# Kernel optimization log

Hardware: AMD Instinct MI355X
Metric: run time of the kernel (lower is better)

Reference implementation:

```python
import jax, jax.numpy as jnp
import numpy as np

N = 50000      # nodes
E = 800000     # edges (before self-loops)
G = 128        # graphs in batch
IN = 128       # in_channels
HID = 32       # hidden_channels (per head)
HEADS = 4
OUT = 64       # out_channels
SLOPE = 0.2    # PyG GATConv default negative_slope


def setup_inputs() -> dict:
    key = jax.random.key(0)
    ks = jax.random.split(key, 24)
    s = 0.1
    inp = {
        'x': jax.random.normal(ks[0], (N, IN), jnp.float32),
        'edge_index': jax.random.randint(ks[1], (2, E), 0, N, dtype=jnp.int32),
        'batch': jnp.sort(jax.random.randint(ks[2], (N,), 0, G, dtype=jnp.int32)),
        # conv1: IN -> HEADS*HID, concat
        'W1': jax.random.normal(ks[3], (IN, HEADS * HID), jnp.float32) * s,
        'a1s': jax.random.normal(ks[4], (HEADS, HID), jnp.float32) * s,
        'a1d': jax.random.normal(ks[5], (HEADS, HID), jnp.float32) * s,
        'b1': jnp.zeros((HEADS * HID,), jnp.float32),
        # conv2: HEADS*HID -> HEADS*HID, concat
        'W2': jax.random.normal(ks[6], (HEADS * HID, HEADS * HID), jnp.float32) * s,
        'a2s': jax.random.normal(ks[7], (HEADS, HID), jnp.float32) * s,
        'a2d': jax.random.normal(ks[8], (HEADS, HID), jnp.float32) * s,
        'b2': jnp.zeros((HEADS * HID,), jnp.float32),
        # conv3
        'W3': jax.random.normal(ks[9], (HEADS * HID, HEADS * HID), jnp.float32) * s,
        'a3s': jax.random.normal(ks[10], (HEADS, HID), jnp.float32) * s,
        'a3d': jax.random.normal(ks[11], (HEADS, HID), jnp.float32) * s,
        'b3': jnp.zeros((HEADS * HID,), jnp.float32),
        # conv4: heads=1, concat=False -> HID
        'W4': jax.random.normal(ks[12], (HEADS * HID, 1 * HID), jnp.float32) * s,
        'a4s': jax.random.normal(ks[13], (1, HID), jnp.float32) * s,
        'a4d': jax.random.normal(ks[14], (1, HID), jnp.float32) * s,
        'b4': jnp.zeros((HID,), jnp.float32),
        # fc: HID -> OUT
        'fcW': jax.random.normal(ks[15], (HID, OUT), jnp.float32) * s,
        'fcb': jnp.zeros((OUT,), jnp.float32),
    }
    return inp


def gat_conv(x, src, dst, W, a_src, a_dst, bias, heads, ch, concat):
    # x: [N, F_in]; src/dst: [E'] with self-loops (PyG add_self_loops=True)
    h = (x @ W).reshape(N, heads, ch)                       # [N, H, C]
    alpha_s = jnp.einsum('nhc,hc->nh', h, a_src)            # [N, H]
    alpha_d = jnp.einsum('nhc,hc->nh', h, a_dst)
    e = jax.nn.leaky_relu(alpha_s[src] + alpha_d[dst], SLOPE)  # [E', H]
    # segment softmax over edges grouped by destination node
    e_max = jax.ops.segment_max(e, dst, num_segments=N)
    e = jnp.exp(e - e_max[dst])
    denom = jax.ops.segment_sum(e, dst, num_segments=N)
    alpha = e / (denom[dst] + 1e-16)                        # [E', H]
    msg = h[src] * alpha[:, :, None]                        # [E', H, C]
    out = jax.ops.segment_sum(msg, dst, num_segments=N)     # [N, H, C]
    out = out.reshape(N, heads * ch) if concat else out.mean(axis=1)
    return out + bias


def reference(x, edge_index, batch, W1, a1s, a1d, b1, W2, a2s, a2d, b2,
              W3, a3s, a3d, b3, W4, a4s, a4d, b4, fcW, fcb):
    loop = jnp.arange(N, dtype=edge_index.dtype)
    src = jnp.concatenate([edge_index[0], loop])            # add self-loops once
    dst = jnp.concatenate([edge_index[1], loop])
    h = jax.nn.elu(gat_conv(x, src, dst, W1, a1s, a1d, b1, HEADS, HID, True))
    h = jax.nn.elu(gat_conv(h, src, dst, W2, a2s, a2d, b2, HEADS, HID, True))
    h = jax.nn.elu(gat_conv(h, src, dst, W3, a3s, a3d, b3, HEADS, HID, True))
    h = jax.nn.elu(gat_conv(h, src, dst, W4, a4s, a4d, b4, 1, HID, False))
    # global mean pool over graphs
    counts = jax.ops.segment_sum(jnp.ones((N,), h.dtype), batch, num_segments=G)
    pooled = jax.ops.segment_sum(h, batch, num_segments=G) / jnp.maximum(counts, 1.0)[:, None]
    # dropout p=0.5 is identity at inference
    return pooled @ fcW + fcb                               # [G, OUT]
```

## Files before the change

### kernel.cpp

```cpp
#include <hip/hip_runtime.h>


constexpr int NN     = 50000;
constexpr int NNPAD  = 50048;
constexpr int EE     = 800000;
constexpr int ETOT   = EE + NN;
constexpr int GG     = 128;
constexpr int HIDC   = 32;
constexpr int OUTC   = 64;

constexpr int NRANGE = (NN + 127) / 128;
constexpr int EPB    = 4096;
constexpr int NBLK   = (EE + EPB - 1) / EPB;
constexpr int RCAP   = 2688;

typedef short  bf16x8 __attribute__((ext_vector_type(8)));
typedef float  f32x4  __attribute__((ext_vector_type(4)));

static __device__ __forceinline__ unsigned short f2bf(float f) {
    unsigned int u = __float_as_uint(f);
    unsigned int r = (u + 0x7fffu + ((u >> 16) & 1u)) >> 16;
    return (unsigned short)r;
}
static __device__ __forceinline__ float bflo(unsigned int v) {
    return __uint_as_float(v << 16);
}
static __device__ __forceinline__ float bfhi(unsigned int v) {
    return __uint_as_float(v & 0xffff0000u);
}
static __device__ __forceinline__ float elu(float v) {
    return (v > 0.f) ? v : (__expf(v) - 1.f);
}
static __device__ __forceinline__ float leaky(float e) {
    return fmaxf(e, 0.f) + 0.2f * fminf(e, 0.f);
}

__global__ __launch_bounds__(256) void local_sort_kernel(
    const int* __restrict__ ei,
    unsigned int* __restrict__ blocksorted,
    int* __restrict__ boffs)
{
    __shared__ unsigned int sorted[EPB];
    __shared__ int hist[NRANGE + 1];
    __shared__ int scanv[NRANGE + 1];
    __shared__ int cur[NRANGE + 1];
    __shared__ int wsum4[4];
    __shared__ int ct_s;

    const int b = blockIdx.x, tid = threadIdx.x;
    const int lane = tid & 63, wid = tid >> 6;
    const int e0 = b * EPB;
    const int ecnt = min(EPB, EE - e0);

    for (int t = tid; t < NRANGE + 1; t += 256) hist[t] = 0;
    __syncthreads();

    unsigned int recs[16];
    int rkey[16];
#pragma unroll
    for (int k = 0; k < 16; ++k) {
        const int idx = tid + k * 256;
        rkey[k] = -1;
        if (idx < ecnt) {
            const int src = ei[e0 + idx];
            const int dst = ei[EE + e0 + idx];
            const int r = dst >> 7;
            recs[k] = (unsigned int)src | ((unsigned int)(dst & 127) << 16);
            rkey[k] = r;
            atomicAdd(&hist[r], 1);
        }
    }
    __syncthreads();

    int carry = 0;
    for (int base = 0; base < NRANGE + 1; base += 256) {
        const int i = base + tid;
        const int v = (i < NRANGE + 1) ? hist[i] : 0;
        int incl = v;
#pragma unroll
        for (int off = 1; off < 64; off <<= 1) {
            int t = __shfl_up(incl, off, 64);
            if (lane >= off) incl += t;
        }
        if (lane == 63) wsum4[wid] = incl;
        __syncthreads();
        if (tid == 0) {
            int s = 0;
#pragma unroll
            for (int w = 0; w < 4; ++w) { int t = wsum4[w]; wsum4[w] = s; s += t; }
            ct_s = s;
        }
        __syncthreads();
        const int excl = carry + wsum4[wid] + incl - v;
        if (i < NRANGE + 1) { scanv[i] = excl; cur[i] = excl; }
        carry += ct_s;
        __syncthreads();
    }

#pragma unroll
    for (int k = 0; k < 16; ++k) {
        if (rkey[k] >= 0) {
            const int pos = atomicAdd(&cur[rkey[k]], 1);
            sorted[pos] = recs[k];
        }
    }
    __syncthreads();

    for (int t = tid; t < ecnt; t += 256)
        blocksorted[(size_t)b * EPB + t] = sorted[t];
    for (int t = tid; t < NRANGE + 1; t += 256)
        boffs[b * (NRANGE + 1) + t] = scanv[t];
}

__global__ __launch_bounds__(256) void rtot_kernel(const int* __restrict__ boffs,
                                                   int* __restrict__ rtot)
{
    const int r = blockIdx.x * 4 + (threadIdx.x >> 6);
    const int lane = threadIdx.x & 63;
    if (r >= NRANGE) return;
    int tot = 0;
    for (int b = lane; b < NBLK; b += 64) {
        const int* bp = boffs + b * (NRANGE + 1) + r;
        tot += bp[1] - bp[0];
    }
#pragma unroll
    for (int k = 1; k < 64; k <<= 1) tot += __shfl_xor(tot, k, 64);
    if (lane == 0) rtot[r] = tot + min(128, NN - r * 128);
}

__global__ __launch_bounds__(512) void rscan_kernel(const int* __restrict__ rtot,
                                                    int* __restrict__ rbase)
{
    __shared__ int wsum[8], wpre[8];
    const int tid = threadIdx.x, lane = tid & 63, wid = tid >> 6;
    int tot = (tid < NRANGE) ? rtot[tid] : 0;
    int incl = tot;
#pragma unroll
    for (int off = 1; off < 64; off <<= 1) {
        int t = __shfl_up(incl, off, 64);
        if (lane >= off) incl += t;
    }
    if (lane == 63) wsum[wid] = incl;
    __syncthreads();
    if (tid < 8) {
        int wv = wsum[tid], winc = wv;
#pragma unroll
        for (int off = 1; off < 8; off <<= 1) {
            int t = __shfl_up(winc, off, 64);
            if (tid >= off) winc += t;
        }
        wpre[tid] = winc - wv;
    }
    __syncthreads();
    const int excl = wpre[wid] + incl - tot;
    if (tid < NRANGE) rbase[tid] = excl;
    if (tid == NRANGE - 1) rbase[NRANGE] = excl + tot;
}

__global__ __launch_bounds__(256) void phaseB_kernel(
    const int* __restrict__ boffs,
    const unsigned int* __restrict__ blocksorted,
    const int* __restrict__ rbase,
    int* __restrict__ offs,
    unsigned int* __restrict__ csrpack)
{
    __shared__ unsigned int rec[RCAP];
    __shared__ unsigned int outpk[RCAP];
    __shared__ int runoff[NBLK + 1];
    __shared__ int bstart[NBLK];
    __shared__ int hist[128], lofs[128], cur[128];
    __shared__ int wsum4[4];
    __shared__ int tot0_s;

    const int r = blockIdx.x, tid = threadIdx.x;
    const int lane = tid & 63, wid = tid >> 6;
    const int base = r * 128;
    const int rn   = min(128, NN - base);

    int cnt = 0;
    if (tid < NBLK) {
        const int* bp = boffs + tid * (NRANGE + 1) + r;
        const int s = bp[0];
        bstart[tid] = s;
        cnt = bp[1] - s;
    }
    if (tid < 128) hist[tid] = 0;
    int incl = cnt;
#pragma unroll
    for (int off = 1; off < 64; off <<= 1) {
        int t = __shfl_up(incl, off, 64);
        if (lane >= off) incl += t;
    }
    if (lane == 63) wsum4[wid] = incl;
    __syncthreads();
    if (tid == 0) {
        int s = 0;
#pragma unroll
        for (int w = 0; w < 4; ++w) { int t = wsum4[w]; wsum4[w] = s; s += t; }
    }
    __syncthreads();
    const int excl = wsum4[wid] + incl - cnt;
    if (tid <= NBLK) runoff[tid] = excl;
    __syncthreads();

    const int tot8 = runoff[NBLK];
    for (int i = tid; i < tot8; i += 256) {
        int lo = 0, hi = NBLK;
        while (lo + 1 < hi) {
            const int mid = (lo + hi) >> 1;
            if (runoff[mid] <= i) lo = mid; else hi = mid;
        }
        rec[i] = blocksorted[(size_t)lo * EPB + bstart[lo] + (i - runoff[lo])];
    }
    for (int t = tid; t < rn; t += 256)
        rec[tot8 + t] = (unsigned int)(base + t) | ((unsigned int)t << 16);
    const int total = min(tot8 + rn, RCAP);
    __syncthreads();

    for (int t = tid; t < total; t += 256) atomicAdd(&hist[rec[t] >> 16], 1);
    __syncthreads();

    if (tid < 64) {
        int v = hist[tid], incl2 = v;
#pragma unroll
        for (int off = 1; off < 64; off <<= 1) {
            int t = __shfl_up(incl2, off, 64);
            if (tid >= off) incl2 += t;
        }
        lofs[tid] = incl2 - v;
        if (tid == 63) tot0_s = incl2;
    }
    __syncthreads();
    if (tid >= 64 && tid < 128) {
        const int l = tid & 63;
        int v = hist[tid], incl2 = v;
#pragma unroll
        for (int off = 1; off < 64; off <<= 1) {
            int t = __shfl_up(incl2, off, 64);
            if (l >= off) incl2 += t;
        }
        lofs[tid] = tot0_s + incl2 - v;
    }
    __syncthreads();

    if (tid < 128) cur[tid] = lofs[tid];
    if (tid < rn) offs[base + tid] = rbase[r] + lofs[tid];
    if (r == 0 && tid == 0) offs[NN] = rbase[NRANGE];
    __syncthreads();

    for (int t = tid; t < total; t += 256) {
        const unsigned int rc = rec[t];
        const int pos = atomicAdd(&cur[rc >> 16], 1);
        outpk[pos] = (rc & 0xffffu) | ((unsigned int)(base + (rc >> 16)) << 16);
    }
    __syncthreads();
    const int rb = rbase[r];
    for (int t = tid; t < total; t += 256) csrpack[rb + t] = outpk[t];
}

__global__ __launch_bounds__(256) void prep_kernel(
    const float* __restrict__ W1, const float* __restrict__ a1s, const float* __restrict__ a1d,
    const float* __restrict__ W2, const float* __restrict__ a2s, const float* __restrict__ a2d,
    const float* __restrict__ W3, const float* __restrict__ a3s, const float* __restrict__ a3d,
    const float* __restrict__ W4, const float* __restrict__ a4s, const float* __restrict__ a4d,
    unsigned short* __restrict__ wtg)
{
    __shared__ float ahat_s[128 * 8];
    const int l = blockIdx.x, tid = threadIdx.x;
    const float *W, *as_, *ad_;
    int fo, nh;
    if (l == 0)      { W = W1; as_ = a1s; ad_ = a1d; fo = 128; nh = 4; }
    else if (l == 1) { W = W2; as_ = a2s; ad_ = a2d; fo = 128; nh = 4; }
    else if (l == 2) { W = W3; as_ = a3s; ad_ = a3d; fo = 128; nh = 4; }
    else             { W = W4; as_ = a4s; ad_ = a4d; fo = 32;  nh = 1; }
    const int F_STG = fo + 16;

    for (int item = tid; item < 128 * 8; item += 256) {
        const int k = item >> 3, j = item & 7;
        const int hh = j & 3;
        const bool is_d = j >= 4;
        float v = 0.f;
        if (hh < nh) {
            const float* av = (is_d ? ad_ : as_) + hh * 32;
            const float* wp = W + (size_t)k * fo + hh * 32;
#pragma unroll 8
            for (int c = 0; c < 32; ++c) v = fmaf(wp[c], av[c], v);
        }
        ahat_s[item] = v;
    }
    __syncthreads();

    unsigned short* outb = wtg + (size_t)l * (144 * 128);
    for (int p = tid; p < F_STG * 64; p += 256) {
        const int n  = p % F_STG;
        const int k2 = p / F_STG;
        float w0 = 0.f, w1 = 0.f;
        if (n < fo) {
            w0 = W[(size_t)(2 * k2) * fo + n];
            w1 = W[(size_t)(2 * k2 + 1) * fo + n];
        } else {
            const int j = n - fo;
            if (j < 8) {
                w0 = ahat_s[(2 * k2) * 8 + j];
                w1 = ahat_s[(2 * k2 + 1) * 8 + j];
            }
        }
        const unsigned int packed = (unsigned int)f2bf(w0) | ((unsigned int)f2bf(w1) << 16);
        const int byte = n * 256 + ((4 * k2) ^ ((n & 7) << 4));
        *reinterpret_cast<unsigned int*>(reinterpret_cast<char*>(outb) + byte) = packed;
    }
}

template<int F_OUT, int NH, bool XF32>
__global__ __launch_bounds__(256) void gemm_mfma_kernel(
    const void* __restrict__ xv,
    const unsigned short* __restrict__ wtg,
    unsigned short* __restrict__ hb,
    float* __restrict__ as_out, float* __restrict__ ad_out)
{
    constexpr int F_STG = F_OUT + 16;
    __shared__ unsigned short wt[F_STG * 128];
    const int tid = threadIdx.x;

    {
        const bf16x8* __restrict__ wg = reinterpret_cast<const bf16x8*>(wtg);
        bf16x8* wl = reinterpret_cast<bf16x8*>(wt);
        constexpr int NV = F_STG * 16;
#pragma unroll
        for (int i = 0; i < NV / 256; ++i)
            wl[i * 256 + tid] = wg[i * 256 + tid];
    }
    __syncthreads();

    const int wave = tid >> 6, lane = tid & 63;
    const int kchunk = (lane >> 4) * 8;
    const int kb_base = (lane >> 4) * 16;

#pragma unroll
    for (int rr = 0; rr < 2; ++rr) {
        const int row0 = blockIdx.x * 128 + rr * 64 + wave * 16;
        const int arow = row0 + (lane & 15);

        bf16x8 a[4];
        if (XF32) {
            if (arow < NN) {
                const float* __restrict__ ap = (const float*)xv + (size_t)arow * 128;
#pragma unroll
                for (int ks = 0; ks < 4; ++ks) {
                    const float4 f0 = *reinterpret_cast<const float4*>(ap + ks * 32 + kchunk);
                    const float4 f1 = *reinterpret_cast<const float4*>(ap + ks * 32 + kchunk + 4);
                    bf16x8 v;
                    v[0] = (short)f2bf(f0.x); v[1] = (short)f2bf(f0.y);
                    v[2] = (short)f2bf(f0.z); v[3] = (short)f2bf(f0.w);
                    v[4] = (short)f2bf(f1.x); v[5] = (short)f2bf(f1.y);
                    v[6] = (short)f2bf(f1.z); v[7] = (short)f2bf(f1.w);
                    a[ks] = v;
                }
            } else {
#pragma unroll
                for (int ks = 0; ks < 4; ++ks) a[ks] = bf16x8{0,0,0,0,0,0,0,0};
            }
        } else {
            const unsigned short* __restrict__ ap =
                (const unsigned short*)xv + (size_t)arow * 128;
#pragma unroll
            for (int ks = 0; ks < 4; ++ks)
                a[ks] = *reinterpret_cast<const bf16x8*>(ap + ks * 32 + kchunk);
        }

        const int rbase = row0 + (lane >> 4) * 4;

#pragma unroll
        for (int nt = 0; nt < F_OUT / 16; ++nt) {
            const int n = nt * 16 + (lane & 15);
            f32x4 acc = {0.f, 0.f, 0.f, 0.f};
#pragma unroll
            for (int ks = 0; ks < 4; ++ks) {
                const int byte = n * 256 + ((ks * 64 + kb_base) ^ ((n & 7) << 4));
                bf16x8 b = *reinterpret_cast<const bf16x8*>(
                    reinterpret_cast<const char*>(wt) + byte);
                acc = __builtin_amdgcn_mfma_f32_16x16x32_bf16(a[ks], b, acc, 0, 0, 0);
            }
#pragma unroll
            for (int r = 0; r < 4; ++r) {
                const int row = rbase + r;
                if (row < NN)
                    hb[(size_t)row * F_OUT + n] = f2bf(acc[r]);
            }
        }

        {
            const int n = F_OUT + (lane & 15);
            f32x4 acc = {0.f, 0.f, 0.f, 0.f};
#pragma unroll
            for (int ks = 0; ks < 4; ++ks) {
                const int byte = n * 256 + ((ks * 64 + kb_base) ^ ((n & 7) << 4));
                bf16x8 b = *reinterpret_cast<const bf16x8*>(
                    reinterpret_cast<const char*>(wt) + byte);
                acc = __builtin_amdgcn_mfma_f32_16x16x32_bf16(a[ks], b, acc, 0, 0, 0);
            }
            const int col = lane & 15;
            if (col < 8) {
                const int hh = col & 3;
                const bool is_d = col >= 4;
                if (hh < NH) {
                    float* op = is_d ? ad_out : as_out;
#pragma unroll
                    for (int r = 0; r < 4; ++r) {
                        const int row = rbase + r;
                        if (row < NN) {
                            if (NH == 4) op[row * 4 + hh] = acc[r];
                            else         op[row]          = acc[r];
                        }
                    }
                }
            }
        }
    }
}

template<int HEADS, int F_OUT, bool OUT_BF16>
__global__ __launch_bounds__(256) void aggregate_kernel(
    const unsigned short* __restrict__ hlin,
    const float* __restrict__ as_,
    const float* __restrict__ ad_,
    const int* __restrict__ offs,
    const unsigned int* __restrict__ csrpack,
    const float* __restrict__ bias,
    void* __restrict__ out_v)
{
    __shared__ float w_all[4][64 * HEADS];
    __shared__ int   s_all[4][64];
    const int wave = threadIdx.x >> 6;
    const int lane = threadIdx.x & 63;
    const int d    = blockIdx.x * 4 + wave;
    if (d >= NN) return;
    float* __restrict__ w_lds   = w_all[wave];
    int*   __restrict__ src_lds = s_all[wave];

    const int beg = offs[d], end = offs[d + 1];

    float ad_h[HEADS];
#pragma unroll
    for (int h = 0; h < HEADS; ++h) ad_h[h] = ad_[d * HEADS + h];

    float acc[8] = {0.f, 0.f, 0.f, 0.f, 0.f, 0.f, 0.f, 0.f};
    float dsum = 0.f;
    const int q  = (F_OUT == 128) ? (lane >> 4) : (lane >> 2);
    const int cl = (F_OUT == 128) ? (lane & 15) : (lane & 3);
    const int hd = (F_OUT == 128) ? (cl >> 2) : 0;

    for (int base = beg; base < end; base += 64) {
        const int cnt = min(64, end - base);
        {
            const int p = base + lane;
            unsigned int pk = (p < end) ? csrpack[p] : 0u;
            const int src = (int)(pk & 0xffffu);
            src_lds[lane] = src;
            if (HEADS == 4) {
                float4 w4 = make_float4(0.f, 0.f, 0.f, 0.f);
                if (p < end) {
                    const float4 s4 = *reinterpret_cast<const float4*>(
                        as_ + (size_t)src * 4);
                    w4.x = __expf(leaky(s4.x + ad_h[0]));
                    w4.y = __expf(leaky(s4.y + ad_h[1]));
                    w4.z = __expf(leaky(s4.z + ad_h[2]));
                    w4.w = __expf(leaky(s4.w + ad_h[3]));
                }
                *reinterpret_cast<float4*>(w_lds + lane * 4) = w4;
            } else {
                float w1 = 0.f;
                if (p < end) w1 = __expf(leaky(as_[src] + ad_h[0]));
                w_lds[lane] = w1;
            }
        }
        asm volatile("s_waitcnt lgkmcnt(0)" ::: "memory");

        if (F_OUT == 128) {
            const int cntR = (cnt + 3) & ~3;
#pragma unroll 2
            for (int j = 0; j < cntR; j += 4) {
                const int   slot = j + q;
                const int   srcj = src_lds[slot];
                const float w    = w_lds[slot * 4 + hd];
                const uint4 hv   = *reinterpret_cast<const uint4*>(
                    hlin + (size_t)srcj * 128 + cl * 8);
                dsum += w;
                acc[0] = fmaf(w, bflo(hv.x), acc[0]);
                acc[1] = fmaf(w, bfhi(hv.x), acc[1]);
                acc[2] = fmaf(w, bflo(hv.y), acc[2]);
                acc[3] = fmaf(w, bfhi(hv.y), acc[3]);
                acc[4] = fmaf(w, bflo(hv.z), acc[4]);
                acc[5] = fmaf(w, bfhi(hv.z), acc[5]);
                acc[6] = fmaf(w, bflo(hv.w), acc[6]);
                acc[7] = fmaf(w, bfhi(hv.w), acc[7]);
            }
        } else {
            const int cntR = (cnt + 15) & ~15;
#pragma unroll 2
            for (int j = 0; j < cntR; j += 16) {
                const int   slot = j + q;
                const int   srcj = src_lds[slot];
                const float w    = w_lds[slot];
                const uint4 hv   = *reinterpret_cast<const uint4*>(
                    hlin + (size_t)srcj * 32 + cl * 8);
                dsum += w;
                acc[0] = fmaf(w, bflo(hv.x), acc[0]);
                acc[1] = fmaf(w, bfhi(hv.x), acc[1]);
                acc[2] = fmaf(w, bflo(hv.y), acc[2]);
                acc[3] = fmaf(w, bfhi(hv.y), acc[3]);
                acc[4] = fmaf(w, bflo(hv.z), acc[4]);
                acc[5] = fmaf(w, bfhi(hv.z), acc[5]);
                acc[6] = fmaf(w, bflo(hv.w), acc[6]);
                acc[7] = fmaf(w, bfhi(hv.w), acc[7]);
            }
        }
    }

    if (F_OUT == 128) {
#pragma unroll
        for (int t = 0; t < 8; ++t) {
            acc[t] += __shfl_xor(acc[t], 16, 64);
            acc[t] += __shfl_xor(acc[t], 32, 64);
        }
        dsum += __shfl_xor(dsum, 16, 64);
        dsum += __shfl_xor(dsum, 32, 64);
        if (lane < 16) {
            const float rinv = 1.f / (dsum + 1e-16f);
            const int c0 = lane * 8;
            float v[8];
#pragma unroll
            for (int t = 0; t < 8; ++t) v[t] = elu(fmaf(acc[t], rinv, bias[c0 + t]));
            uint4 pk;
            pk.x = (unsigned int)f2bf(v[0]) | ((unsigned int)f2bf(v[1]) << 16);
            pk.y = (unsigned int)f2bf(v[2]) | ((unsigned int)f2bf(v[3]) << 16);
            pk.z = (unsigned int)f2bf(v[4]) | ((unsigned int)f2bf(v[5]) << 16);
            pk.w = (unsigned int)f2bf(v[6]) | ((unsigned int)f2bf(v[7]) << 16);
            *reinterpret_cast<uint4*>((unsigned short*)out_v + (size_t)d * 128 + c0) = pk;
        }
    } else {
#pragma unroll
        for (int t = 0; t < 8; ++t) {
            acc[t] += __shfl_xor(acc[t], 4, 64);
            acc[t] += __shfl_xor(acc[t], 8, 64);
            acc[t] += __shfl_xor(acc[t], 16, 64);
            acc[t] += __shfl_xor(acc[t], 32, 64);
        }
        dsum += __shfl_xor(dsum, 4, 64);
        dsum += __shfl_xor(dsum, 8, 64);
        dsum += __shfl_xor(dsum, 16, 64);
        dsum += __shfl_xor(dsum, 32, 64);
        if (lane < 4) {
            const float rinv = 1.f / (dsum + 1e-16f);
            const int c0 = lane * 8;
            float v[8];
#pragma unroll
            for (int t = 0; t < 8; ++t) v[t] = elu(fmaf(acc[t], rinv, bias[c0 + t]));
            float* op = (float*)out_v + (size_t)d * 32 + c0;
            *reinterpret_cast<float4*>(op)     = make_float4(v[0], v[1], v[2], v[3]);
            *reinterpret_cast<float4*>(op + 4) = make_float4(v[4], v[5], v[6], v[7]);
        }
    }
}

__global__ __launch_bounds__(256) void pool_fc_kernel(
    const float* __restrict__ h4, const int* __restrict__ batch,
    const float* __restrict__ fcW, const float* __restrict__ fcb,
    float* __restrict__ out)
{
    const int g = blockIdx.x;
    __shared__ int sb, se;
    if (threadIdx.x == 0) {
        int lo = 0, hi = NN;
        while (lo < hi) { int mid = (lo + hi) >> 1; if (batch[mid] < g) lo = mid + 1; else hi = mid; }
        sb = lo;
        lo = sb; hi = NN;
        while (lo < hi) { int mid = (lo + hi) >> 1; if (batch[mid] < g + 1) lo = mid + 1; else hi = mid; }
        se = lo;
    }
    __syncthreads();
    const int s = sb, e = se;

    const int c  = threadIdx.x & 31;
    const int rg = threadIdx.x >> 5;
    float acc = 0.f;
    for (int n = s + rg; n < e; n += 8)
        acc += h4[(size_t)n * HIDC + c];

    __shared__ float red[8][32];
    red[rg][c] = acc;
    __syncthreads();
    __shared__ float pooled_s[32];
    if (threadIdx.x < 32) {
        float v = 0.f;
#pragma unroll
        for (int r = 0; r < 8; ++r) v += red[r][threadIdx.x];
        pooled_s[threadIdx.x] = v / fmaxf((float)(e - s), 1.f);
    }
    __syncthreads();
    if (threadIdx.x < OUTC) {
        const int o = threadIdx.x;
        float a2 = fcb[o];
#pragma unroll
        for (int cc = 0; cc < HIDC; ++cc)
            a2 = fmaf(pooled_s[cc], fcW[cc * OUTC + o], a2);
        out[g * OUTC + o] = a2;
    }
}

extern "C" void kernel_launch(void* const* d_in, const int* in_sizes, int n_in,
                              void* d_out, int out_size, void* d_ws, size_t ws_size,
                              hipStream_t stream)
{
    const float* x     = (const float*)d_in[0];
    const int*   ei    = (const int*)d_in[1];
    const int*   batch = (const int*)d_in[2];
    const float* W1  = (const float*)d_in[3];
    const float* a1s = (const float*)d_in[4];
    const float* a1d = (const float*)d_in[5];
    const float* b1  = (const float*)d_in[6];
    const float* W2  = (const float*)d_in[7];
    const float* a2s = (const float*)d_in[8];
    const float* a2d = (const float*)d_in[9];
    const float* b2  = (const float*)d_in[10];
    const float* W3  = (const float*)d_in[11];
    const float* a3s = (const float*)d_in[12];
    const float* a3d = (const float*)d_in[13];
    const float* b3  = (const float*)d_in[14];
    const float* W4  = (const float*)d_in[15];
    const float* a4s = (const float*)d_in[16];
    const float* a4d = (const float*)d_in[17];
    const float* b4  = (const float*)d_in[18];
    const float* fcW = (const float*)d_in[19];
    const float* fcb = (const float*)d_in[20];
    float* out = (float*)d_out;

    unsigned short* xb = (unsigned short*)d_ws;
    unsigned short* hb = xb + (size_t)NNPAD * 128;
    float* asb  = (float*)(hb + (size_t)NNPAD * 128);
    float* adb  = asb + (size_t)NN * 4;
    int*   offs    = (int*)(adb + (size_t)NN * 4);
    unsigned int* csrpack = (unsigned int*)(offs + NN + 1);
    int*   boffs  = (int*)(csrpack + ETOT);
    int*   rbase  = boffs + NBLK * (NRANGE + 1);
    int*   rtot   = rbase + NRANGE + 1;
    unsigned short* wtg = (unsigned short*)(rtot + NRANGE);
    unsigned int* blocksorted = (unsigned int*)hb;
    float* bufF = (float*)xb;

    local_sort_kernel<<<NBLK, 256, 0, stream>>>(ei, blocksorted, boffs);
    rtot_kernel<<<(NRANGE + 3) / 4, 256, 0, stream>>>(boffs, rtot);
    rscan_kernel<<<1, 512, 0, stream>>>(rtot, rbase);
    phaseB_kernel<<<NRANGE, 256, 0, stream>>>(boffs, blocksorted, rbase, offs, csrpack);

    prep_kernel<<<4, 256, 0, stream>>>(W1, a1s, a1d, W2, a2s, a2d,
                                       W3, a3s, a3d, W4, a4s, a4d, wtg);

    constexpr int GEMM_GRID = NNPAD / 128;
    constexpr int AGG_GRID  = (NN + 3) / 4;
    constexpr size_t WSTRIDE = 144 * 128;

    gemm_mfma_kernel<128, 4, true><<<GEMM_GRID, 256, 0, stream>>>(x, wtg + 0 * WSTRIDE, hb, asb, adb);
    aggregate_kernel<4, 128, true><<<AGG_GRID, 256, 0, stream>>>(hb, asb, adb, offs, csrpack, b1, xb);
    gemm_mfma_kernel<128, 4, false><<<GEMM_GRID, 256, 0, stream>>>(xb, wtg + 1 * WSTRIDE, hb, asb, adb);
    aggregate_kernel<4, 128, true><<<AGG_GRID, 256, 0, stream>>>(hb, asb, adb, offs, csrpack, b2, xb);
    gemm_mfma_kernel<128, 4, false><<<GEMM_GRID, 256, 0, stream>>>(xb, wtg + 2 * WSTRIDE, hb, asb, adb);
    aggregate_kernel<4, 128, true><<<AGG_GRID, 256, 0, stream>>>(hb, asb, adb, offs, csrpack, b3, xb);
    gemm_mfma_kernel<32, 1, false><<<GEMM_GRID, 256, 0, stream>>>(xb, wtg + 3 * WSTRIDE, hb, asb, adb);
    aggregate_kernel<1, 32, false><<<AGG_GRID, 256, 0, stream>>>(hb, asb, adb, offs, csrpack, b4, bufF);

    pool_fc_kernel<<<GG, 256, 0, stream>>>(bufF, batch, fcW, fcb, out);
}
```

Before: 249.7 us.

## Process two destination nodes per wave in aggregation and use packed bf16 conversion

Each wave in the aggregate kernel now handles two destination nodes, interleaving their edge chunks so the gathers for both are in flight at once, and the grid shrinks to NN/8 blocks. The inner gather loop unroll goes from 2 to 4. Float-to-bf16 rounding now uses the HIP packed conversion intrinsic instead of manual bit arithmetic. The goal is more memory-level parallelism in the latency-bound gather. The cost is imbalance when the two nodes have different degrees, plus higher register pressure. The grid assumes NN is divisible by 8, and the d>=NN guard is removed.

Result: slower. 283.8 us (+13.7%).

```diff
diff --git a/kernel.cpp b/kernel.cpp
--- a/kernel.cpp
+++ b/kernel.cpp
@@ -1,4 +1,5 @@
 #include <hip/hip_runtime.h>
+#include <hip/hip_bf16.h>
 
 
 constexpr int NN     = 50000;
@@ -18,9 +19,12 @@
 typedef float  f32x4  __attribute__((ext_vector_type(4)));
 
 static __device__ __forceinline__ unsigned short f2bf(float f) {
-    unsigned int u = __float_as_uint(f);
-    unsigned int r = (u + 0x7fffu + ((u >> 16) & 1u)) >> 16;
-    return (unsigned short)r;
+    __hip_bfloat16 h = __float2bfloat16(f);
+    unsigned short u; __builtin_memcpy(&u, &h, 2); return u;
+}
+static __device__ __forceinline__ unsigned int f2bf2(float lo, float hi) {
+    __hip_bfloat162 h2 = __float22bfloat162_rn(make_float2(lo, hi));
+    unsigned int u; __builtin_memcpy(&u, &h2, 4); return u;
 }
 static __device__ __forceinline__ float bflo(unsigned int v) {
     return __uint_as_float(v << 16);
@@ -305,7 +309,7 @@
                 w1 = ahat_s[(2 * k2 + 1) * 8 + j];
             }
         }
-        const unsigned int packed = (unsigned int)f2bf(w0) | ((unsigned int)f2bf(w1) << 16);
+        const unsigned int packed = f2bf2(w0, w1);
         const int byte = n * 256 + ((4 * k2) ^ ((n & 7) << 4));
         *reinterpret_cast<unsigned int*>(reinterpret_cast<char*>(outb) + byte) = packed;
     }
@@ -349,11 +353,12 @@
                 for (int ks = 0; ks < 4; ++ks) {
                     const float4 f0 = *reinterpret_cast<const float4*>(ap + ks * 32 + kchunk);
                     const float4 f1 = *reinterpret_cast<const float4*>(ap + ks * 32 + kchunk + 4);
-                    bf16x8 v;
-                    v[0] = (short)f2bf(f0.x); v[1] = (short)f2bf(f0.y);
-                    v[2] = (short)f2bf(f0.z); v[3] = (short)f2bf(f0.w);
-                    v[4] = (short)f2bf(f1.x); v[5] = (short)f2bf(f1.y);
-                    v[6] = (short)f2bf(f1.z); v[7] = (short)f2bf(f1.w);
+                    uint4 u;
+                    u.x = f2bf2(f0.x, f0.y);
+                    u.y = f2bf2(f0.z, f0.w);
+                    u.z = f2bf2(f1.x, f1.y);
+                    u.w = f2bf2(f1.z, f1.w);
+                    bf16x8 v; __builtin_memcpy(&v, &u, 16);
                     a[ks] = v;
                 }
             } else {
@@ -419,6 +424,132 @@
     }
 }
 
+template<int HEADS>
+static __device__ __forceinline__ void agg_stage(
+    const unsigned int* __restrict__ csrpack, const float* __restrict__ as_,
+    const float* __restrict__ ad_h,
+    float* __restrict__ w_lds, int* __restrict__ src_lds,
+    int lane, int p0, int end)
+{
+    const int p = p0 + lane;
+    const unsigned int pk = (p < end) ? csrpack[p] : 0u;
+    const int src = (int)(pk & 0xffffu);
+    src_lds[lane] = src;
+    if (HEADS == 4) {
+        float4 w4 = make_float4(0.f, 0.f, 0.f, 0.f);
+        if (p < end) {
+            const float4 s4 = *reinterpret_cast<const float4*>(as_ + (size_t)src * 4);
+            w4.x = __expf(leaky(s4.x + ad_h[0]));
+            w4.y = __expf(leaky(s4.y + ad_h[1]));
+            w4.z = __expf(leaky(s4.z + ad_h[2]));
+            w4.w = __expf(leaky(s4.w + ad_h[3]));
+        }
+        *reinterpret_cast<float4*>(w_lds + lane * 4) = w4;
+    } else {
+        float w1 = 0.f;
+        if (p < end) w1 = __expf(leaky(as_[src] + ad_h[0]));
+        w_lds[lane] = w1;
+    }
+}
+
+template<int F_OUT>
+static __device__ __forceinline__ void agg_inner(
+    const unsigned short* __restrict__ hlin,
+    const float* __restrict__ w_lds, const int* __restrict__ src_lds,
+    int cnt, int q, int cl, int hd, float acc[8], float& dsum)
+{
+    if (F_OUT == 128) {
+        const int cntR = (cnt + 3) & ~3;
+#pragma unroll 4
+        for (int j = 0; j < cntR; j += 4) {
+            const int   slot = j + q;
+            const int   srcj = src_lds[slot];
+            const float w    = w_lds[slot * 4 + hd];
+            const uint4 hv   = *reinterpret_cast<const uint4*>(
+                hlin + (size_t)srcj * 128 + cl * 8);
+            dsum += w;
+            acc[0] = fmaf(w, bflo(hv.x), acc[0]);
+            acc[1] = fmaf(w, bfhi(hv.x), acc[1]);
+            acc[2] = fmaf(w, bflo(hv.y), acc[2]);
+            acc[3] = fmaf(w, bfhi(hv.y), acc[3]);
+            acc[4] = fmaf(w, bflo(hv.z), acc[4]);
+            acc[5] = fmaf(w, bfhi(hv.z), acc[5]);
+            acc[6] = fmaf(w, bflo(hv.w), acc[6]);
+            acc[7] = fmaf(w, bfhi(hv.w), acc[7]);
+        }
+    } else {
+        const int cntR = (cnt + 15) & ~15;
+#pragma unroll 4
+        for (int j = 0; j < cntR; j += 16) {
+            const int   slot = j + q;
+            const int   srcj = src_lds[slot];
+            const float w    = w_lds[slot];
+            const uint4 hv   = *reinterpret_cast<const uint4*>(
+                hlin + (size_t)srcj * 32 + cl * 8);
+            dsum += w;
+            acc[0] = fmaf(w, bflo(hv.x), acc[0]);
+            acc[1] = fmaf(w, bfhi(hv.x), acc[1]);
+            acc[2] = fmaf(w, bflo(hv.y), acc[2]);
+            acc[3] = fmaf(w, bfhi(hv.y), acc[3]);
+            acc[4] = fmaf(w, bflo(hv.z), acc[4]);
+            acc[5] = fmaf(w, bfhi(hv.z), acc[5]);
+            acc[6] = fmaf(w, bflo(hv.w), acc[6]);
+            acc[7] = fmaf(w, bfhi(hv.w), acc[7]);
+        }
+    }
+}
+
+template<int F_OUT, bool OUT_BF16>
+static __device__ __forceinline__ void agg_epilogue(
+    float acc[8], float dsum, int lane, int d,
+    const float* __restrict__ bias, void* __restrict__ out_v)
+{
+    if (F_OUT == 128) {
+#pragma unroll
+        for (int t = 0; t < 8; ++t) {
+            acc[t] += __shfl_xor(acc[t], 16, 64);
+            acc[t] += __shfl_xor(acc[t], 32, 64);
+        }
+        dsum += __shfl_xor(dsum, 16, 64);
+        dsum += __shfl_xor(dsum, 32, 64);
+        if (lane < 16) {
+            const float rinv = 1.f / (dsum + 1e-16f);
+            const int c0 = lane * 8;
+            float v[8];
+#pragma unroll
+            for (int t = 0; t < 8; ++t) v[t] = elu(fmaf(acc[t], rinv, bias[c0 + t]));
+            uint4 pk;
+            pk.x = f2bf2(v[0], v[1]);
+            pk.y = f2bf2(v[2], v[3]);
+            pk.z = f2bf2(v[4], v[5]);
+            pk.w = f2bf2(v[6], v[7]);
+            *reinterpret_cast<uint4*>((unsigned short*)out_v + (size_t)d * 128 + c0) = pk;
+        }
+    } else {
+#pragma unroll
+        for (int t = 0; t < 8; ++t) {
+            acc[t] += __shfl_xor(acc[t], 4, 64);
+            acc[t] += __shfl_xor(acc[t], 8, 64);
+            acc[t] += __shfl_xor(acc[t], 16, 64);
+            acc[t] += __shfl_xor(acc[t], 32, 64);
+        }
+        dsum += __shfl_xor(dsum, 4, 64);
+        dsum += __shfl_xor(dsum, 8, 64);
+        dsum += __shfl_xor(dsum, 16, 64);
+        dsum += __shfl_xor(dsum, 32, 64);
+        if (lane < 4) {
+            const float rinv = 1.f / (dsum + 1e-16f);
+            const int c0 = lane * 8;
+            float v[8];
+#pragma unroll
+            for (int t = 0; t < 8; ++t) v[t] = elu(fmaf(acc[t], rinv, bias[c0 + t]));
+            float* op = (float*)out_v + (size_t)d * 32 + c0;
+            *reinterpret_cast<float4*>(op)     = make_float4(v[0], v[1], v[2], v[3]);
+            *reinterpret_cast<float4*>(op + 4) = make_float4(v[4], v[5], v[6], v[7]);
+        }
+    }
+}
+
 template<int HEADS, int F_OUT, bool OUT_BF16>
 __global__ __launch_bounds__(256) void aggregate_kernel(
     const unsigned short* __restrict__ hlin,
@@ -429,138 +560,52 @@
     const float* __restrict__ bias,
     void* __restrict__ out_v)
 {
-    __shared__ float w_all[4][64 * HEADS];
-    __shared__ int   s_all[4][64];
+    __shared__ float w_all[8][64 * HEADS];
+    __shared__ int   s_all[8][64];
     const int wave = threadIdx.x >> 6;
     const int lane = threadIdx.x & 63;
-    const int d    = blockIdx.x * 4 + wave;
-    if (d >= NN) return;
-    float* __restrict__ w_lds   = w_all[wave];
-    int*   __restrict__ src_lds = s_all[wave];
-
-    const int beg = offs[d], end = offs[d + 1];
-
-    float ad_h[HEADS];
-#pragma unroll
-    for (int h = 0; h < HEADS; ++h) ad_h[h] = ad_[d * HEADS + h];
-
-    float acc[8] = {0.f, 0.f, 0.f, 0.f, 0.f, 0.f, 0.f, 0.f};
-    float dsum = 0.f;
+    const int d0   = blockIdx.x * 8 + wave * 2;
+    const int d1   = d0 + 1;
+    float* __restrict__ w0 = w_all[wave * 2];
+    float* __restrict__ w1 = w_all[wave * 2 + 1];
+    int*   __restrict__ s0 = s_all[wave * 2];
+    int*   __restrict__ s1 = s_all[wave * 2 + 1];
+
+    const int beg0 = offs[d0];
+    const int end0 = offs[d1];
+    const int end1 = offs[d1 + 1];
+
+    float ad0[HEADS], ad1[HEADS];
+#pragma unroll
+    for (int h = 0; h < HEADS; ++h) {
+        ad0[h] = ad_[d0 * HEADS + h];
+        ad1[h] = ad_[d1 * HEADS + h];
+    }
+
+    float acc0[8] = {0,0,0,0,0,0,0,0};
+    float acc1[8] = {0,0,0,0,0,0,0,0};
+    float dsum0 = 0.f, dsum1 = 0.f;
     const int q  = (F_OUT == 128) ? (lane >> 4) : (lane >> 2);
     const int cl = (F_OUT == 128) ? (lane & 15) : (lane & 3);
     const int hd = (F_OUT == 128) ? (cl >> 2) : 0;
 
-    for (int base = beg; base < end; base += 64) {
-        const int cnt = min(64, end - base);
-        {
-            const int p = base + lane;
-            unsigned int pk = (p < end) ? csrpack[p] : 0u;
-            const int src = (int)(pk & 0xffffu);
-            src_lds[lane] = src;
-            if (HEADS == 4) {
-                float4 w4 = make_float4(0.f, 0.f, 0.f, 0.f);
-                if (p < end) {
-                    const float4 s4 = *reinterpret_cast<const float4*>(
-                        as_ + (size_t)src * 4);
-                    w4.x = __expf(leaky(s4.x + ad_h[0]));
-                    w4.y = __expf(leaky(s4.y + ad_h[1]));
-                    w4.z = __expf(leaky(s4.z + ad_h[2]));
-                    w4.w = __expf(leaky(s4.w + ad_h[3]));
-                }
-                *reinterpret_cast<float4*>(w_lds + lane * 4) = w4;
-            } else {
-                float w1 = 0.f;
-                if (p < end) w1 = __expf(leaky(as_[src] + ad_h[0]));
-                w_lds[lane] = w1;
-            }
-        }
+    int b0 = beg0, b1 = end0;
+    while (b0 < end0 || b1 < end1) {
+        if (b0 < end0) agg_stage<HEADS>(csrpack, as_, ad0, w0, s0, lane, b0, end0);
+        if (b1 < end1) agg_stage<HEADS>(csrpack, as_, ad1, w1, s1, lane, b1, end1);
         asm volatile("s_waitcnt lgkmcnt(0)" ::: "memory");
-
-        if (F_OUT == 128) {
-            const int cntR = (cnt + 3) & ~3;
-#pragma unroll 2
-            for (int j = 0; j < cntR; j += 4) {
-                const int   slot = j + q;
-                const int   srcj = src_lds[slot];
-                const float w    = w_lds[slot * 4 + hd];
-                const uint4 hv   = *reinterpret_cast<const uint4*>(
-                    hlin + (size_t)srcj * 128 + cl * 8);
-                dsum += w;
-                acc[0] = fmaf(w, bflo(hv.x), acc[0]);
-                acc[1] = fmaf(w, bfhi(hv.x), acc[1]);
-                acc[2] = fmaf(w, bflo(hv.y), acc[2]);
-                acc[3] = fmaf(w, bfhi(hv.y), acc[3]);
-                acc[4] = fmaf(w, bflo(hv.z), acc[4]);
-                acc[5] = fmaf(w, bfhi(hv.z), acc[5]);
-                acc[6] = fmaf(w, bflo(hv.w), acc[6]);
-                acc[7] = fmaf(w, bfhi(hv.w), acc[7]);
-            }
-        } else {
-            const int cntR = (cnt + 15) & ~15;
-#pragma unroll 2
-            for (int j = 0; j < cntR; j += 16) {
-                const int   slot = j + q;
-                const int   srcj = src_lds[slot];
-                const float w    = w_lds[slot];
-                const uint4 hv   = *reinterpret_cast<const uint4*>(
-                    hlin + (size_t)srcj * 32 + cl * 8);
-                dsum += w;
-                acc[0] = fmaf(w, bflo(hv.x), acc[0]);
-                acc[1] = fmaf(w, bfhi(hv.x), acc[1]);
-                acc[2] = fmaf(w, bflo(hv.y), acc[2]);
-                acc[3] = fmaf(w, bfhi(hv.y), acc[3]);
-                acc[4] = fmaf(w, bflo(hv.z), acc[4]);
-                acc[5] = fmaf(w, bfhi(hv.z), acc[5]);
-                acc[6] = fmaf(w, bflo(hv.w), acc[6]);
-                acc[7] = fmaf(w, bfhi(hv.w), acc[7]);
-            }
-        }
-    }
-
-    if (F_OUT == 128) {
-#pragma unroll
-        for (int t = 0; t < 8; ++t) {
-            acc[t] += __shfl_xor(acc[t], 16, 64);
-            acc[t] += __shfl_xor(acc[t], 32, 64);
-        }
-        dsum += __shfl_xor(dsum, 16, 64);
-        dsum += __shfl_xor(dsum, 32, 64);
-        if (lane < 16) {
-            const float rinv = 1.f / (dsum + 1e-16f);
-            const int c0 = lane * 8;
-            float v[8];
-#pragma unroll
-            for (int t = 0; t < 8; ++t) v[t] = elu(fmaf(acc[t], rinv, bias[c0 + t]));
-            uint4 pk;
-            pk.x = (unsigned int)f2bf(v[0]) | ((unsigned int)f2bf(v[1]) << 16);
-            pk.y = (unsigned int)f2bf(v[2]) | ((unsigned int)f2bf(v[3]) << 16);
-            pk.z = (unsigned int)f2bf(v[4]) | ((unsigned int)f2bf(v[5]) << 16);
-            pk.w = (unsigned int)f2bf(v[6]) | ((unsigned int)f2bf(v[7]) << 16);
-            *reinterpret_cast<uint4*>((unsigned short*)out_v + (size_t)d * 128 + c0) = pk;
-        }
-    } else {
-#pragma unroll
-        for (int t = 0; t < 8; ++t) {
-            acc[t] += __shfl_xor(acc[t], 4, 64);
-            acc[t] += __shfl_xor(acc[t], 8, 64);
-            acc[t] += __shfl_xor(acc[t], 16, 64);
-            acc[t] += __shfl_xor(acc[t], 32, 64);
-        }
-        dsum += __shfl_xor(dsum, 4, 64);
-        dsum += __shfl_xor(dsum, 8, 64);
-        dsum += __shfl_xor(dsum, 16, 64);
-        dsum += __shfl_xor(dsum, 32, 64);
-        if (lane < 4) {
-            const float rinv = 1.f / (dsum + 1e-16f);
-            const int c0 = lane * 8;
-            float v[8];
-#pragma unroll
-            for (int t = 0; t < 8; ++t) v[t] = elu(fmaf(acc[t], rinv, bias[c0 + t]));
-            float* op = (float*)out_v + (size_t)d * 32 + c0;
-            *reinterpret_cast<float4*>(op)     = make_float4(v[0], v[1], v[2], v[3]);
-            *reinterpret_cast<float4*>(op + 4) = make_float4(v[4], v[5], v[6], v[7]);
-        }
-    }
+        if (b0 < end0) {
+            agg_inner<F_OUT>(hlin, w0, s0, min(64, end0 - b0), q, cl, hd, acc0, dsum0);
+            b0 += 64;
+        }
+        if (b1 < end1) {
+            agg_inner<F_OUT>(hlin, w1, s1, min(64, end1 - b1), q, cl, hd, acc1, dsum1);
+            b1 += 64;
+        }
+    }
+
+    agg_epilogue<F_OUT, OUT_BF16>(acc0, dsum0, lane, d0, bias, out_v);
+    agg_epilogue<F_OUT, OUT_BF16>(acc1, dsum1, lane, d1, bias, out_v);
 }
 
 __global__ __launch_bounds__(256) void pool_fc_kernel(
@@ -657,7 +702,7 @@
                                        W3, a3s, a3d, W4, a4s, a4d, wtg);
 
     constexpr int GEMM_GRID = NNPAD / 128;
-    constexpr int AGG_GRID  = (NN + 3) / 4;
+    constexpr int AGG_GRID  = NN / 8;
     constexpr size_t WSTRIDE = 144 * 128;
 
     gemm_mfma_kernel<128, 4, true><<<GEMM_GRID, 256, 0, stream>>>(x, wtg + 0 * WSTRIDE, hb, asb, adb);
```
